# Kernel optimization log

Hardware: AMD Instinct MI355X
Metric: run time of the kernel (lower is better)

## Reference

```python
import jax, jax.numpy as jnp
import numpy as np

NEG = jnp.float32(-1e30)  # finite stand-in for -inf in masked max
SLOPE = 0.01              # F.leaky_relu default negative slope


def _lrelu(v):
    return jnp.where(v >= 0, v, SLOPE * v)


def _mlp(pts, w1, b1, w2, b2, w3, b3):
    # pts: [2, N] -> [64, N]; 1x1 Conv1d == pointwise linear over channel dim
    z = _lrelu(w1 @ pts + b1[:, None])
    z = _lrelu(w2 @ z + b2[:, None])
    z = _lrelu(w3 @ z + b3[:, None])
    return z


def setup_inputs() -> dict:
    key = jax.random.key(0)
    ks = jax.random.split(key, 10)
    B, C, H, W = 4, 19, 256, 256
    x = jax.random.randint(ks[0], (B, C, H, W), 0, 2, dtype=jnp.int32)
    # grid exactly as in the torch module: meshgrid of two linspaces, flattened
    g = np.array(np.meshgrid(np.linspace(-1, 1, 256), np.linspace(-1, 1, 256),
                             sparse=False)).astype(np.float32)  # [2,256,256]
    grid = jnp.asarray(g.reshape(2, -1))  # [2, 65536]
    w1 = jax.random.normal(ks[1], (64, 2), jnp.float32) * 0.5
    b1 = jax.random.normal(ks[2], (64,), jnp.float32) * 0.1
    w2 = jax.random.normal(ks[3], (64, 64), jnp.float32) * 0.125
    b2 = jax.random.normal(ks[4], (64,), jnp.float32) * 0.1
    w3 = jax.random.normal(ks[5], (64, 64), jnp.float32) * 0.125
    b3 = jax.random.normal(ks[6], (64,), jnp.float32) * 0.1
    fcw = jax.random.normal(ks[7], (512, 64 * C), jnp.float32)
    fcb = jax.random.normal(ks[8], (512,), jnp.float32) * 0.1
    return {"x": x, "grid": grid, "w1": w1, "b1": b1, "w2": w2, "b2": b2,
            "w3": w3, "b3": b3, "fcw": fcw, "fcb": fcb}


def reference(x, grid, w1, b1, w2, b2, w3, b3, fcw, fcb):
    B, C = x.shape[0], x.shape[1]
    # Pointwise MLP on the shared grid once (grid identical for all b,c)
    feats = _mlp(grid, w1, b1, w2, b2, w3, b3)                 # [64, N]
    # Fallback feature for empty masks: MLP on a single zero point
    zero_feat = _mlp(jnp.zeros((2, 1), feats.dtype),
                     w1, b1, w2, b2, w3, b3)[:, 0]             # [64]
    mask = (x.reshape(B, C, -1) == 1)                          # [B, C, N]
    # Masked max over the ragged point sets, fully vectorized
    masked = jnp.where(mask[:, :, None, :], feats[None, None], NEG)
    z = jnp.max(masked, axis=-1)                               # [B, C, 64]
    empty = ~jnp.any(mask, axis=-1)                            # [B, C]
    z = jnp.where(empty[..., None], zero_feat, z)
    flat = z.reshape(B, C * 64)                                # channel-major cat
    # EqualLinear: weight scaled by 1/sqrt(in_dim) (lr_mul=1)
    scale = jnp.float32(1.0 / np.sqrt(C * 64))
    out = flat @ (fcw * scale).T + fcb                         # [B, 512]
    return jnp.repeat(out[:, None, :], 18, axis=1)             # [B, 18, 512]
```

## Files before the change

kernel.cpp:

```cpp
#include <hip/hip_runtime.h>

#define NPTS  65536
#define NBC   76
#define NREP  8
#define KEYN  4864

typedef _Float16 f16;
typedef __fp16   h16x2 __attribute__((ext_vector_type(2)));
typedef _Float16 f16x8 __attribute__((ext_vector_type(8)));
typedef float    f32x4 __attribute__((ext_vector_type(4)));

__device__ __forceinline__ float lrelu(float v) { return fmaxf(v, 0.01f * v); }

__device__ __forceinline__ unsigned pkrtz(float lo, float hi) {
  h16x2 p = __builtin_amdgcn_cvt_pkrtz(lo, hi);
  return __builtin_bit_cast(unsigned, p);
}
__device__ __forceinline__ unsigned pkey(unsigned u) {
  unsigned t = (u >> 15) & 0x00010001u;
  return u ^ (0x80008000u | (t * 0x7FFFu));
}
__device__ __forceinline__ unsigned pkmax(unsigned a, unsigned b) {
  unsigned d;
  asm("v_pk_max_u16 %0, %1, %2" : "=v"(d) : "v"(a), "v"(b));
  return d;
}
__device__ __forceinline__ unsigned sext1(unsigned x, int b) {
  return (unsigned)(((int)(x << (31 - b))) >> 31);
}

__global__ __launch_bounds__(512, 8) void kA_mlp(
    const float* __restrict__ grid,
    const float* __restrict__ w1, const float* __restrict__ b1,
    const float* __restrict__ w2, const float* __restrict__ b2,
    const float* __restrict__ w3, const float* __restrict__ b3,
    unsigned* __restrict__ kbuf)
{
  __shared__ __align__(16) unsigned char smem[36864];
  f16* zA  = (f16*)(smem);
  f16* zB  = (f16*)(smem + 9216);
  f16* wf2 = (f16*)(smem + 18432);
  f16* wf3 = (f16*)(smem + 27648);

  const int t    = threadIdx.x;
  const int lane = t & 63;
  const int wv   = t >> 6;
  const int n0   = blockIdx.x * 64;

  float g0 = grid[n0 + lane], g1 = grid[NPTS + n0 + lane];

  {
    int ch = t >> 3, k0 = (t & 7) * 8;
    const float4* s2 = (const float4*)(w2 + ch * 64 + k0);
    float4 a = s2[0], b = s2[1];
    *(uint4*)&wf2[ch * 72 + k0] =
        make_uint4(pkrtz(a.x, a.y), pkrtz(a.z, a.w), pkrtz(b.x, b.y), pkrtz(b.z, b.w));
    const float4* s3 = (const float4*)(w3 + ch * 64 + k0);
    float4 c = s3[0], d = s3[1];
    *(uint4*)&wf3[ch * 72 + k0] =
        make_uint4(pkrtz(c.x, c.y), pkrtz(c.z, c.w), pkrtz(d.x, d.y), pkrtz(d.z, d.w));
  }

  {
    unsigned uo[4];
    #pragma unroll
    for (int p = 0; p < 4; ++p) {
      int j = wv * 8 + p * 2;
      float z0 = lrelu(w1[2 * j] * g0 + w1[2 * j + 1] * g1 + b1[j]);
      float z1 = lrelu(w1[2 * j + 2] * g0 + w1[2 * j + 3] * g1 + b1[j + 1]);
      uo[p] = pkrtz(z0, z1);
    }
    *(uint4*)&zA[lane * 72 + wv * 8] = make_uint4(uo[0], uo[1], uo[2], uo[3]);
  }
  __syncthreads();

  const int chb = (wv & 3) * 16, pth = (wv >> 2) * 32;
  const int c15 = lane & 15, q = lane >> 4;
  const int chq = chb + q * 4;
  const int pt0 = pth + c15, pt1 = pth + 16 + c15;

  f32x4 acc0, acc1;

  {
    float4 bias = *(const float4*)(b2 + chq);
    acc0 = (f32x4){bias.x, bias.y, bias.z, bias.w};
    acc1 = acc0;
    #pragma unroll
    for (int k0 = 0; k0 < 64; k0 += 32) {
      f16x8 af = *(const f16x8*)&wf2[(chb + c15) * 72 + k0 + q * 8];
      f16x8 b0 = *(const f16x8*)&zA[pt0 * 72 + k0 + q * 8];
      f16x8 b1f = *(const f16x8*)&zA[pt1 * 72 + k0 + q * 8];
      acc0 = __builtin_amdgcn_mfma_f32_16x16x32_f16(af, b0, acc0, 0, 0, 0);
      acc1 = __builtin_amdgcn_mfma_f32_16x16x32_f16(af, b1f, acc1, 0, 0, 0);
    }
    *(uint2*)&zB[pt0 * 72 + chq] =
        make_uint2(pkrtz(lrelu(acc0[0]), lrelu(acc0[1])),
                   pkrtz(lrelu(acc0[2]), lrelu(acc0[3])));
    *(uint2*)&zB[pt1 * 72 + chq] =
        make_uint2(pkrtz(lrelu(acc1[0]), lrelu(acc1[1])),
                   pkrtz(lrelu(acc1[2]), lrelu(acc1[3])));
  }
  __syncthreads();

  {
    float4 bias = *(const float4*)(b3 + chq);
    acc0 = (f32x4){bias.x, bias.y, bias.z, bias.w};
    acc1 = acc0;
    #pragma unroll
    for (int k0 = 0; k0 < 64; k0 += 32) {
      f16x8 af = *(const f16x8*)&wf3[(chb + c15) * 72 + k0 + q * 8];
      f16x8 b0 = *(const f16x8*)&zB[pt0 * 72 + k0 + q * 8];
      f16x8 b1f = *(const f16x8*)&zB[pt1 * 72 + k0 + q * 8];
      acc0 = __builtin_amdgcn_mfma_f32_16x16x32_f16(af, b0, acc0, 0, 0, 0);
      acc1 = __builtin_amdgcn_mfma_f32_16x16x32_f16(af, b1f, acc1, 0, 0, 0);
    }
    unsigned* kb = kbuf + (unsigned)blockIdx.x * 2048;
    int r0 = chq >> 1;
    kb[r0 * 64 + pt0]       = pkey(pkrtz(lrelu(acc0[0]), lrelu(acc0[1])));
    kb[(r0 + 1) * 64 + pt0] = pkey(pkrtz(lrelu(acc0[2]), lrelu(acc0[3])));
    kb[r0 * 64 + pt1]       = pkey(pkrtz(lrelu(acc1[0]), lrelu(acc1[1])));
    kb[(r0 + 1) * 64 + pt1] = pkey(pkrtz(lrelu(acc1[2]), lrelu(acc1[3])));
  }
}

__global__ __launch_bounds__(512, 8) void kB_max(
    const int* __restrict__ x, const unsigned* __restrict__ kbuf,
    unsigned* __restrict__ keys)
{
  __shared__ unsigned zk[32 * 68];
  __shared__ unsigned long long mbits[NBC];

  const int t    = threadIdx.x;
  const int lane = t & 63;
  const int wv   = t >> 6;
  const int n0   = blockIdx.x * 64;

  const uint4 kv = *(const uint4*)(kbuf + (unsigned)blockIdx.x * 2048 + t * 4);

  int xv[10];
  #pragma unroll
  for (int i = 0; i < 10; ++i) {
    int bc = wv + 8 * i;
    xv[i] = (bc < NBC) ? x[(bc << 16) + n0 + lane] : 0;
  }

  *(uint4*)&zk[(t >> 4) * 68 + (t & 15) * 4] = kv;

  #pragma unroll
  for (int i = 0; i < 10; ++i) {
    int bc = wv + 8 * i;
    unsigned long long m = __ballot(xv[i] == 1);
    if (bc < NBC && lane == 0) mbits[bc] = m;
  }
  __syncthreads();

  const int rw = t & 31, bg = t >> 5;
  const int bc0 = bg * 5;

  unsigned mlo[5], mhi[5], uacc[5];
  #pragma unroll
  for (int ii = 0; ii < 5; ++ii) {
    int bc = bc0 + ii;
    unsigned long long m = (bc < NBC) ? mbits[bc] : 0ull;
    mlo[ii] = (unsigned)m;
    mhi[ii] = (unsigned)(m >> 32);
    uacc[ii] = 0u;
  }

  #pragma unroll
  for (int np = 0; np < 16; ++np) {
    uint4 z4 = *(const uint4*)&zk[rw * 68 + np * 4];
    const int p = np * 4, pb = p & 31;
    #pragma unroll
    for (int ii = 0; ii < 5; ++ii) {
      unsigned m = (p < 32) ? mlo[ii] : mhi[ii];
      unsigned s0 = sext1(m, pb),     s1 = sext1(m, pb + 1);
      unsigned s2 = sext1(m, pb + 2), s3 = sext1(m, pb + 3);
      unsigned a = uacc[ii];
      a = pkmax(a, z4.x & s0); a = pkmax(a, z4.y & s1);
      a = pkmax(a, z4.z & s2); a = pkmax(a, z4.w & s3);
      uacc[ii] = a;
    }
  }

  unsigned* krep = keys + (blockIdx.x & (NREP - 1)) * KEYN;
  #pragma unroll
  for (int ii = 0; ii < 5; ++ii) {
    int bc = bc0 + ii;
    if (bc < NBC) {
      unsigned lo = uacc[ii] & 0xFFFFu, hi = uacc[ii] >> 16;
      if (lo) atomicMax(&krep[bc * 64 + 2 * rw], lo);
      if (hi) atomicMax(&krep[bc * 64 + 2 * rw + 1], hi);
    }
  }
}

__global__ __launch_bounds__(256) void k2_fc(
    const unsigned* __restrict__ keys,
    const float* __restrict__ b1, const float* __restrict__ w2,
    const float* __restrict__ b2, const float* __restrict__ w3,
    const float* __restrict__ b3,
    const float* __restrict__ fcw, const float* __restrict__ fcb,
    float* __restrict__ out)
{
  __shared__ float flat[4864];
  __shared__ float za[64], zb[64], zf[64];
  const int t = threadIdx.x;

  if (t < 64) za[t] = lrelu(b1[t]);
  __syncthreads();
  if (t < 64) {
    float s = b2[t];
    #pragma unroll 8
    for (int k = 0; k < 64; ++k) s += w2[t * 64 + k] * za[k];
    zb[t] = lrelu(s);
  }
  __syncthreads();
  if (t < 64) {
    float s = b3[t];
    #pragma unroll 8
    for (int k = 0; k < 64; ++k) s += w3[t * 64 + k] * zb[k];
    zf[t] = lrelu(s);
  }
  __syncthreads();

  for (int idx = t; idx < 4864; idx += 256) {
    unsigned m = keys[idx];
    #pragma unroll
    for (int r = 1; r < NREP; ++r) m = max(m, keys[r * KEYN + idx]);
    float v;
    if (m) {
      unsigned u = (m & 0x8000u) ? (m ^ 0x8000u) : (~m & 0xFFFFu);
      unsigned short us = (unsigned short)u;
      v = (float)__builtin_bit_cast(f16, us);
    } else {
      v = zf[idx & 63];
    }
    flat[idx] = v;
  }
  __syncthreads();

  const int wv = t >> 6, lane = t & 63;
  const int o = blockIdx.x * 4 + wv;
  const float* wrow = fcw + o * 1216;
  float fa0 = 0.f, fa1 = 0.f, fa2 = 0.f, fa3 = 0.f;
  #pragma unroll
  for (int i = 0; i < 19; ++i) {
    int jj = i * 64 + lane;
    float wvv = wrow[jj];
    fa0 += wvv * flat[jj];
    fa1 += wvv * flat[1216 + jj];
    fa2 += wvv * flat[2432 + jj];
    fa3 += wvv * flat[3648 + jj];
  }
  #pragma unroll
  for (int off = 32; off > 0; off >>= 1) {
    fa0 += __shfl_xor(fa0, off);
    fa1 += __shfl_xor(fa1, off);
    fa2 += __shfl_xor(fa2, off);
    fa3 += __shfl_xor(fa3, off);
  }
  const float scale = 0.028676966733820225f;
  float cb = fcb[o];
  if (lane < 18) {
    out[(0 * 18 + lane) * 512 + o] = fa0 * scale + cb;
    out[(1 * 18 + lane) * 512 + o] = fa1 * scale + cb;
    out[(2 * 18 + lane) * 512 + o] = fa2 * scale + cb;
    out[(3 * 18 + lane) * 512 + o] = fa3 * scale + cb;
  }
}

extern "C" void kernel_launch(void* const* d_in, const int* in_sizes, int n_in,
                              void* d_out, int out_size, void* d_ws, size_t ws_size,
                              hipStream_t stream)
{
  const int*   x    = (const int*)d_in[0];
  const float* grid = (const float*)d_in[1];
  const float* w1   = (const float*)d_in[2];
  const float* b1   = (const float*)d_in[3];
  const float* w2   = (const float*)d_in[4];
  const float* b2   = (const float*)d_in[5];
  const float* w3   = (const float*)d_in[6];
  const float* b3   = (const float*)d_in[7];
  const float* fcw  = (const float*)d_in[8];
  const float* fcb  = (const float*)d_in[9];
  float* out = (float*)d_out;

  unsigned* keys = (unsigned*)d_ws;
  unsigned* kbuf = (unsigned*)d_ws + 65536;

  (void)hipMemsetAsync(d_ws, 0, NREP * KEYN * sizeof(unsigned), stream);
  hipLaunchKernelGGL(kA_mlp, dim3(1024), dim3(512), 0, stream,
                     grid, w1, b1, w2, b2, w3, b3, kbuf);
  hipLaunchKernelGGL(kB_max, dim3(1024), dim3(512), 0, stream,
                     x, kbuf, keys);
  hipLaunchKernelGGL(k2_fc, dim3(128), dim3(256), 0, stream,
                     keys, b1, w2, b2, w3, b3, fcw, fcb, out);
}
```

Measured before the change: 132.7 us.

## Process two 64-point tiles per block in MLP and max kernels

Result: faster. 126.7 us (-4.6%).

```diff
diff --git a/kernel.cpp b/kernel.cpp
--- a/kernel.cpp
+++ b/kernel.cpp
@@ -29,25 +29,60 @@
   return (unsigned)(((int)(x << (31 - b))) >> 31);
 }
 
-__global__ __launch_bounds__(512, 8) void kA_mlp(
+__device__ __forceinline__ void mfma_layer(
+    const f16* __restrict__ A, const f16* __restrict__ B,
+    const float* __restrict__ bias,
+    int chb, int c15, int q, int pt0, int pt1,
+    f32x4& acc0, f32x4& acc1)
+{
+  float4 bv = *(const float4*)(bias + chb + q * 4);
+  acc0 = (f32x4){bv.x, bv.y, bv.z, bv.w};
+  acc1 = acc0;
+  #pragma unroll
+  for (int k0 = 0; k0 < 64; k0 += 32) {
+    f16x8 af = *(const f16x8*)&A[(chb + c15) * 72 + k0 + q * 8];
+    f16x8 b0 = *(const f16x8*)&B[pt0 * 72 + k0 + q * 8];
+    f16x8 b1 = *(const f16x8*)&B[pt1 * 72 + k0 + q * 8];
+    acc0 = __builtin_amdgcn_mfma_f32_16x16x32_f16(af, b0, acc0, 0, 0, 0);
+    acc1 = __builtin_amdgcn_mfma_f32_16x16x32_f16(af, b1, acc1, 0, 0, 0);
+  }
+}
+
+__device__ __forceinline__ void layer1(
+    f16* __restrict__ zA, const float* __restrict__ w1,
+    const float* __restrict__ b1, int wv, int lane, float g0, float g1)
+{
+  unsigned uo[4];
+  #pragma unroll
+  for (int p = 0; p < 4; ++p) {
+    int j = wv * 8 + p * 2;
+    float z0 = lrelu(w1[2 * j] * g0 + w1[2 * j + 1] * g1 + b1[j]);
+    float z1 = lrelu(w1[2 * j + 2] * g0 + w1[2 * j + 3] * g1 + b1[j + 1]);
+    uo[p] = pkrtz(z0, z1);
+  }
+  *(uint4*)&zA[lane * 72 + wv * 8] = make_uint4(uo[0], uo[1], uo[2], uo[3]);
+}
+
+__global__ __launch_bounds__(512, 4) void kA_mlp(
     const float* __restrict__ grid,
     const float* __restrict__ w1, const float* __restrict__ b1,
     const float* __restrict__ w2, const float* __restrict__ b2,
     const float* __restrict__ w3, const float* __restrict__ b3,
     unsigned* __restrict__ kbuf)
 {
-  __shared__ __align__(16) unsigned char smem[36864];
-  f16* zA  = (f16*)(smem);
-  f16* zB  = (f16*)(smem + 9216);
-  f16* wf2 = (f16*)(smem + 18432);
-  f16* wf3 = (f16*)(smem + 27648);
-
-  const int t    = threadIdx.x;
-  const int lane = t & 63;
-  const int wv   = t >> 6;
-  const int n0   = blockIdx.x * 64;
-
-  float g0 = grid[n0 + lane], g1 = grid[NPTS + n0 + lane];
+  __shared__ __align__(16) unsigned char smem[55296];
+  f16* zA0 = (f16*)(smem);
+  f16* zA1 = (f16*)(smem + 9216);
+  f16* zB0 = (f16*)(smem + 18432);
+  f16* zB1 = (f16*)(smem + 27648);
+  f16* wf2 = (f16*)(smem + 36864);
+  f16* wf3 = (f16*)(smem + 46080);
+
+  const int t = threadIdx.x, lane = t & 63, wv = t >> 6;
+  const int n0 = blockIdx.x * 128;
+
+  float g0a = grid[n0 + lane],      g1a = grid[NPTS + n0 + lane];
+  float g0b = grid[n0 + 64 + lane], g1b = grid[NPTS + n0 + 64 + lane];
 
   {
     int ch = t >> 3, k0 = (t & 7) * 8;
@@ -60,113 +95,60 @@
     *(uint4*)&wf3[ch * 72 + k0] =
         make_uint4(pkrtz(c.x, c.y), pkrtz(c.z, c.w), pkrtz(d.x, d.y), pkrtz(d.z, d.w));
   }
-
-  {
-    unsigned uo[4];
-    #pragma unroll
-    for (int p = 0; p < 4; ++p) {
-      int j = wv * 8 + p * 2;
-      float z0 = lrelu(w1[2 * j] * g0 + w1[2 * j + 1] * g1 + b1[j]);
-      float z1 = lrelu(w1[2 * j + 2] * g0 + w1[2 * j + 3] * g1 + b1[j + 1]);
-      uo[p] = pkrtz(z0, z1);
-    }
-    *(uint4*)&zA[lane * 72 + wv * 8] = make_uint4(uo[0], uo[1], uo[2], uo[3]);
-  }
+  layer1(zA0, w1, b1, wv, lane, g0a, g1a);
   __syncthreads();
 
   const int chb = (wv & 3) * 16, pth = (wv >> 2) * 32;
   const int c15 = lane & 15, q = lane >> 4;
   const int chq = chb + q * 4;
   const int pt0 = pth + c15, pt1 = pth + 16 + c15;
-
-  f32x4 acc0, acc1;
-
-  {
-    float4 bias = *(const float4*)(b2 + chq);
-    acc0 = (f32x4){bias.x, bias.y, bias.z, bias.w};
-    acc1 = acc0;
-    #pragma unroll
-    for (int k0 = 0; k0 < 64; k0 += 32) {
-      f16x8 af = *(const f16x8*)&wf2[(chb + c15) * 72 + k0 + q * 8];
-      f16x8 b0 = *(const f16x8*)&zA[pt0 * 72 + k0 + q * 8];
-      f16x8 b1f = *(const f16x8*)&zA[pt1 * 72 + k0 + q * 8];
-      acc0 = __builtin_amdgcn_mfma_f32_16x16x32_f16(af, b0, acc0, 0, 0, 0);
-      acc1 = __builtin_amdgcn_mfma_f32_16x16x32_f16(af, b1f, acc1, 0, 0, 0);
-    }
-    *(uint2*)&zB[pt0 * 72 + chq] =
-        make_uint2(pkrtz(lrelu(acc0[0]), lrelu(acc0[1])),
-                   pkrtz(lrelu(acc0[2]), lrelu(acc0[3])));
-    *(uint2*)&zB[pt1 * 72 + chq] =
-        make_uint2(pkrtz(lrelu(acc1[0]), lrelu(acc1[1])),
-                   pkrtz(lrelu(acc1[2]), lrelu(acc1[3])));
-  }
-  __syncthreads();
-
-  {
-    float4 bias = *(const float4*)(b3 + chq);
-    acc0 = (f32x4){bias.x, bias.y, bias.z, bias.w};
-    acc1 = acc0;
-    #pragma unroll
-    for (int k0 = 0; k0 < 64; k0 += 32) {
-      f16x8 af = *(const f16x8*)&wf3[(chb + c15) * 72 + k0 + q * 8];
-      f16x8 b0 = *(const f16x8*)&zB[pt0 * 72 + k0 + q * 8];
-      f16x8 b1f = *(const f16x8*)&zB[pt1 * 72 + k0 + q * 8];
-      acc0 = __builtin_amdgcn_mfma_f32_16x16x32_f16(af, b0, acc0, 0, 0, 0);
-      acc1 = __builtin_amdgcn_mfma_f32_16x16x32_f16(af, b1f, acc1, 0, 0, 0);
-    }
-    unsigned* kb = kbuf + (unsigned)blockIdx.x * 2048;
-    int r0 = chq >> 1;
-    kb[r0 * 64 + pt0]       = pkey(pkrtz(lrelu(acc0[0]), lrelu(acc0[1])));
-    kb[(r0 + 1) * 64 + pt0] = pkey(pkrtz(lrelu(acc0[2]), lrelu(acc0[3])));
-    kb[r0 * 64 + pt1]       = pkey(pkrtz(lrelu(acc1[0]), lrelu(acc1[1])));
-    kb[(r0 + 1) * 64 + pt1] = pkey(pkrtz(lrelu(acc1[2]), lrelu(acc1[3])));
-  }
-}
-
-__global__ __launch_bounds__(512, 8) void kB_max(
-    const int* __restrict__ x, const unsigned* __restrict__ kbuf,
-    unsigned* __restrict__ keys)
-{
-  __shared__ unsigned zk[32 * 68];
-  __shared__ unsigned long long mbits[NBC];
-
-  const int t    = threadIdx.x;
-  const int lane = t & 63;
-  const int wv   = t >> 6;
-  const int n0   = blockIdx.x * 64;
-
-  const uint4 kv = *(const uint4*)(kbuf + (unsigned)blockIdx.x * 2048 + t * 4);
-
-  int xv[10];
-  #pragma unroll
-  for (int i = 0; i < 10; ++i) {
-    int bc = wv + 8 * i;
-    xv[i] = (bc < NBC) ? x[(bc << 16) + n0 + lane] : 0;
-  }
-
-  *(uint4*)&zk[(t >> 4) * 68 + (t & 15) * 4] = kv;
-
-  #pragma unroll
-  for (int i = 0; i < 10; ++i) {
-    int bc = wv + 8 * i;
-    unsigned long long m = __ballot(xv[i] == 1);
-    if (bc < NBC && lane == 0) mbits[bc] = m;
-  }
-  __syncthreads();
-
-  const int rw = t & 31, bg = t >> 5;
-  const int bc0 = bg * 5;
-
-  unsigned mlo[5], mhi[5], uacc[5];
-  #pragma unroll
-  for (int ii = 0; ii < 5; ++ii) {
-    int bc = bc0 + ii;
-    unsigned long long m = (bc < NBC) ? mbits[bc] : 0ull;
-    mlo[ii] = (unsigned)m;
-    mhi[ii] = (unsigned)(m >> 32);
-    uacc[ii] = 0u;
-  }
-
+  const int r0 = chq >> 1;
+
+  {
+    f32x4 a0, a1;
+    mfma_layer(wf2, zA0, b2, chb, c15, q, pt0, pt1, a0, a1);
+    *(uint2*)&zB0[pt0 * 72 + chq] =
+        make_uint2(pkrtz(lrelu(a0[0]), lrelu(a0[1])), pkrtz(lrelu(a0[2]), lrelu(a0[3])));
+    *(uint2*)&zB0[pt1 * 72 + chq] =
+        make_uint2(pkrtz(lrelu(a1[0]), lrelu(a1[1])), pkrtz(lrelu(a1[2]), lrelu(a1[3])));
+  }
+  layer1(zA1, w1, b1, wv, lane, g0b, g1b);
+  __syncthreads();
+
+  {
+    f32x4 c0, c1;
+    mfma_layer(wf3, zB0, b3, chb, c15, q, pt0, pt1, c0, c1);
+    unsigned* kb = kbuf + (unsigned)(blockIdx.x * 2) * 2048;
+    kb[r0 * 64 + pt0]       = pkey(pkrtz(lrelu(c0[0]), lrelu(c0[1])));
+    kb[(r0 + 1) * 64 + pt0] = pkey(pkrtz(lrelu(c0[2]), lrelu(c0[3])));
+    kb[r0 * 64 + pt1]       = pkey(pkrtz(lrelu(c1[0]), lrelu(c1[1])));
+    kb[(r0 + 1) * 64 + pt1] = pkey(pkrtz(lrelu(c1[2]), lrelu(c1[3])));
+  }
+  {
+    f32x4 a0, a1;
+    mfma_layer(wf2, zA1, b2, chb, c15, q, pt0, pt1, a0, a1);
+    *(uint2*)&zB1[pt0 * 72 + chq] =
+        make_uint2(pkrtz(lrelu(a0[0]), lrelu(a0[1])), pkrtz(lrelu(a0[2]), lrelu(a0[3])));
+    *(uint2*)&zB1[pt1 * 72 + chq] =
+        make_uint2(pkrtz(lrelu(a1[0]), lrelu(a1[1])), pkrtz(lrelu(a1[2]), lrelu(a1[3])));
+  }
+  __syncthreads();
+
+  {
+    f32x4 c0, c1;
+    mfma_layer(wf3, zB1, b3, chb, c15, q, pt0, pt1, c0, c1);
+    unsigned* kb = kbuf + (unsigned)(blockIdx.x * 2 + 1) * 2048;
+    kb[r0 * 64 + pt0]       = pkey(pkrtz(lrelu(c0[0]), lrelu(c0[1])));
+    kb[(r0 + 1) * 64 + pt0] = pkey(pkrtz(lrelu(c0[2]), lrelu(c0[3])));
+    kb[r0 * 64 + pt1]       = pkey(pkrtz(lrelu(c1[0]), lrelu(c1[1])));
+    kb[(r0 + 1) * 64 + pt1] = pkey(pkrtz(lrelu(c1[2]), lrelu(c1[3])));
+  }
+}
+
+__device__ __forceinline__ void phaseB(
+    const unsigned* __restrict__ zk, const unsigned* mlo, const unsigned* mhi,
+    unsigned* uacc, int rw)
+{
   #pragma unroll
   for (int np = 0; np < 16; ++np) {
     uint4 z4 = *(const uint4*)&zk[rw * 68 + np * 4];
@@ -182,6 +164,76 @@
       uacc[ii] = a;
     }
   }
+}
+
+__global__ __launch_bounds__(512, 8) void kB_max(
+    const int* __restrict__ x, const unsigned* __restrict__ kbuf,
+    unsigned* __restrict__ keys)
+{
+  __shared__ unsigned zk0[32 * 68], zk1[32 * 68];
+  __shared__ unsigned long long mb0[NBC], mb1[NBC];
+
+  const int t = threadIdx.x, lane = t & 63, wv = t >> 6;
+  const int n0 = blockIdx.x * 128;
+
+  uint4 kv0 = *(const uint4*)(kbuf + (unsigned)(blockIdx.x * 2) * 2048 + t * 4);
+  uint4 kv1 = *(const uint4*)(kbuf + (unsigned)(blockIdx.x * 2 + 1) * 2048 + t * 4);
+
+  *(uint4*)&zk0[(t >> 4) * 68 + (t & 15) * 4] = kv0;
+
+  {
+    int xa[10];
+    #pragma unroll
+    for (int i = 0; i < 10; ++i) {
+      int bc = wv + 8 * i;
+      if (bc < NBC) xa[i] = x[(bc << 16) + n0 + lane];
+    }
+    #pragma unroll
+    for (int i = 0; i < 10; ++i) {
+      int bc = wv + 8 * i;
+      if (bc < NBC) {
+        unsigned long long m = __ballot(xa[i] == 1);
+        if (lane == 0) mb0[bc] = m;
+      }
+    }
+    #pragma unroll
+    for (int i = 0; i < 10; ++i) {
+      int bc = wv + 8 * i;
+      if (bc < NBC) xa[i] = x[(bc << 16) + n0 + 64 + lane];
+    }
+    #pragma unroll
+    for (int i = 0; i < 10; ++i) {
+      int bc = wv + 8 * i;
+      if (bc < NBC) {
+        unsigned long long m = __ballot(xa[i] == 1);
+        if (lane == 0) mb1[bc] = m;
+      }
+    }
+  }
+  __syncthreads();
+  *(uint4*)&zk1[(t >> 4) * 68 + (t & 15) * 4] = kv1;
+
+  const int rw = t & 31, bg = t >> 5;
+  const int bc0 = bg * 5;
+
+  unsigned uacc[5] = {0u, 0u, 0u, 0u, 0u};
+  unsigned mlo[5], mhi[5];
+
+  #pragma unroll
+  for (int ii = 0; ii < 5; ++ii) {
+    int bc = bc0 + ii;
+    unsigned long long m = (bc < NBC) ? mb0[bc] : 0ull;
+    mlo[ii] = (unsigned)m; mhi[ii] = (unsigned)(m >> 32);
+  }
+  phaseB(zk0, mlo, mhi, uacc, rw);
+  __syncthreads();
+  #pragma unroll
+  for (int ii = 0; ii < 5; ++ii) {
+    int bc = bc0 + ii;
+    unsigned long long m = (bc < NBC) ? mb1[bc] : 0ull;
+    mlo[ii] = (unsigned)m; mhi[ii] = (unsigned)(m >> 32);
+  }
+  phaseB(zk1, mlo, mhi, uacc, rw);
 
   unsigned* krep = keys + (blockIdx.x & (NREP - 1)) * KEYN;
   #pragma unroll
@@ -290,9 +342,9 @@
   unsigned* kbuf = (unsigned*)d_ws + 65536;
 
   (void)hipMemsetAsync(d_ws, 0, NREP * KEYN * sizeof(unsigned), stream);
-  hipLaunchKernelGGL(kA_mlp, dim3(1024), dim3(512), 0, stream,
+  hipLaunchKernelGGL(kA_mlp, dim3(512), dim3(512), 0, stream,
                      grid, w1, b1, w2, b2, w3, b3, kbuf);
-  hipLaunchKernelGGL(kB_max, dim3(1024), dim3(512), 0, stream,
+  hipLaunchKernelGGL(kB_max, dim3(512), dim3(512), 0, stream,
                      x, kbuf, keys);
   hipLaunchKernelGGL(k2_fc, dim3(128), dim3(256), 0, stream,
                      keys, b1, w2, b2, w3, b3, fcw, fcb, out);
```
